# Optimization experiments

Measured on AMD Instinct MI355X. Metric: run time of the kernel, lower is better.

The kernel has to match this reference:

```python
import jax, jax.numpy as jnp
import numpy as np

N = 50000
E = 1600000
IN_DIM = 128
HIDDEN = 128


def setup_inputs() -> dict:
    key = jax.random.key(0)
    ks = jax.random.split(key, 10)
    s = lambda d: 1.0 / np.sqrt(d)
    return {
        "x": jax.random.normal(ks[0], (N, IN_DIM), dtype=jnp.float32),
        "edge_index": jax.random.randint(ks[1], (2, E), 0, N, dtype=jnp.int64),
        "w1l": jax.random.normal(ks[2], (HIDDEN, IN_DIM), dtype=jnp.float32) * s(IN_DIM),
        "b1l": jnp.zeros((HIDDEN,), dtype=jnp.float32),
        "w1r": jax.random.normal(ks[3], (HIDDEN, IN_DIM), dtype=jnp.float32) * s(IN_DIM),
        "w2l": jax.random.normal(ks[4], (HIDDEN, HIDDEN), dtype=jnp.float32) * s(HIDDEN),
        "b2l": jnp.zeros((HIDDEN,), dtype=jnp.float32),
        "w2r": jax.random.normal(ks[5], (HIDDEN, HIDDEN), dtype=jnp.float32) * s(HIDDEN),
        "mw1": jax.random.normal(ks[6], (HIDDEN, HIDDEN), dtype=jnp.float32) * s(HIDDEN),
        "mb1": jnp.zeros((HIDDEN,), dtype=jnp.float32),
        "mw2": jax.random.normal(ks[7], (1, HIDDEN), dtype=jnp.float32) * s(HIDDEN),
        "mb2": jnp.zeros((1,), dtype=jnp.float32),
    }


def _mean_aggr(x, src, dst, num_nodes):
    # scatter-mean of source features onto target nodes (PyG SAGEConv mean aggr)
    summed = jax.ops.segment_sum(x[src], dst, num_segments=num_nodes)  # [N, D]
    count = jax.ops.segment_sum(jnp.ones((src.shape[0],), x.dtype), dst,
                                num_segments=num_nodes)
    return summed / jnp.maximum(count, 1.0)[:, None]


def _sage_conv(x, src, dst, wl, bl, wr):
    # out = lin_l(mean_aggr(x_neighbors)) + lin_r(x_root)
    aggr = _mean_aggr(x, src, dst, x.shape[0])
    return aggr @ wl.T + bl + x @ wr.T


def reference(x, edge_index, w1l, b1l, w1r, w2l, b2l, w2r, mw1, mb1, mw2, mb2):
    src, dst = edge_index[0], edge_index[1]
    h = jax.nn.relu(_sage_conv(x, src, dst, w1l, b1l, w1r))   # dropout: eval mode
    h = jax.nn.relu(_sage_conv(h, src, dst, w2l, b2l, w2r))
    h = jax.nn.relu(h @ mw1.T + mb1)
    logits = (h @ mw2.T + mb2).squeeze(-1)                    # [N]
    return logits
```

## Files before the change

### kernel.cpp

```cpp
#include <hip/hip_runtime.h>
#include <hip/hip_bf16.h>
#include <cstdint>

#define HD 128
#define BKSZ 256
#define BCAP 12288

typedef __attribute__((ext_vector_type(8))) short bfx8;
typedef __attribute__((ext_vector_type(4))) float fx4;

__device__ inline float bf2f(short s) {
    union { uint32_t u; float f; } c;
    c.u = ((uint32_t)(unsigned short)s) << 16;
    return c.f;
}
__device__ inline unsigned short f2bf(float v) {
    union { float f; uint32_t u; } c;
    c.f = v;
    uint32_t u = c.u + 0x7FFF + ((c.u >> 16) & 1);
    return (unsigned short)(u >> 16);
}

__device__ inline void stage_lds(const void* g, void* l, int nbytes) {
    const char* gc = (const char*)g;
    for (int off = threadIdx.x * 16; off < nbytes; off += 4096) {
        __builtin_amdgcn_global_load_lds(
            (const __attribute__((address_space(1))) unsigned int*)(gc + off),
            (__attribute__((address_space(3))) unsigned int*)
                ((__attribute__((address_space(3))) char*)l + off),
            16, 0, 0);
    }
}


__global__ void k_zero(int* __restrict__ p, int n) {
    int i = blockIdx.x * 256 + threadIdx.x;
    if (i < n) p[i] = 0;
}

__global__ __launch_bounds__(256) void k_bin(const int* __restrict__ ei, int E, int NBK,
                                             int* __restrict__ bcnt,
                                             int* __restrict__ bpack) {
    __shared__ int lhist[BKSZ];
    __shared__ int gbase[BKSZ];
    int base = blockIdx.x * 4096;

    for (int i = threadIdx.x; i < NBK; i += 256) lhist[i] = 0;
    __syncthreads();

    int pw[16];
    int meta[16];
    const int4* s4 = (const int4*)ei;
    const int4* d4 = (const int4*)(ei + E);
    int c0 = base >> 2;
    int EC = E >> 2;
#pragma unroll
    for (int j = 0; j < 4; ++j) {
        int c4 = c0 + j * 256 + threadIdx.x;
        bool ok = (c4 < EC);
        int4 sv = make_int4(0, 0, 0, 0), dv = make_int4(0, 0, 0, 0);
        if (ok) { sv = s4[c4]; dv = d4[c4]; }
        int ss[4] = {sv.x, sv.y, sv.z, sv.w};
        int dd[4] = {dv.x, dv.y, dv.z, dv.w};
#pragma unroll
        for (int l = 0; l < 4; ++l) {
            int idx = j * 4 + l;
            meta[idx] = -1;
            if (ok) {
                int d = dd[l];
                int b = d >> 8;
                int lr = atomicAdd(&lhist[b], 1);
                pw[idx]   = ((d & 255) << 24) | ss[l];
                meta[idx] = (b << 16) | lr;
            }
        }
    }
    __syncthreads();
    for (int i = threadIdx.x; i < NBK; i += 256) {
        int c = lhist[i];
        gbase[i] = c ? atomicAdd(&bcnt[i], c) : 0;
    }
    __syncthreads();
#pragma unroll
    for (int idx = 0; idx < 16; ++idx) {
        int m = meta[idx];
        if (m >= 0) {
            int b = m >> 16, lr = m & 0xFFFF;
            int pos = b * BCAP + min(gbase[b] + lr, BCAP - 1);
            bpack[pos] = pw[idx];
        }
    }
}

__global__ __launch_bounds__(1024) void k_bscan(const int* __restrict__ bcnt,
                                                int* __restrict__ boff, int NBK, int E) {
    __shared__ int sh[1024];
    int t = threadIdx.x;
    int v = (t < NBK) ? bcnt[t] : 0;
    sh[t] = v;
    __syncthreads();
    for (int d = 1; d < 1024; d <<= 1) {
        int o = (t >= d) ? sh[t - d] : 0;
        __syncthreads();
        sh[t] += o;
        __syncthreads();
    }
    if (t < NBK) boff[t] = sh[t] - v;
    if (t == 0) boff[NBK] = E;
}

__global__ __launch_bounds__(256) void k_bucket(const int* __restrict__ bpack,
                                                const int* __restrict__ bcnt,
                                                const int* __restrict__ boff,
                                                int* __restrict__ offsets,
                                                int* __restrict__ sorted,
                                                int N, int E) {
    __shared__ int lh[BKSZ];
    __shared__ int cur[BKSZ];
    __shared__ int wsum[4];
    int b = blockIdx.x;
    int cnt = min(bcnt[b], BCAP);
    int base = b * BCAP;
    int obase = boff[b];
    int tid = threadIdx.x;

    lh[tid] = 0;
    __syncthreads();
    for (int i = tid; i < cnt; i += 256)
        atomicAdd(&lh[((unsigned)bpack[base + i]) >> 24], 1);
    __syncthreads();

    int v = lh[tid];
    int sum = v;
#pragma unroll
    for (int s = 1; s < 64; s <<= 1) {
        int o = __shfl_up(sum, s, 64);
        if ((tid & 63) >= s) sum += o;
    }
    int wid = tid >> 6;
    if ((tid & 63) == 63) wsum[wid] = sum;
    __syncthreads();
    int prefix = 0;
#pragma unroll
    for (int w = 0; w < 4; ++w)
        if (w < wid) prefix += wsum[w];
    int excl = prefix + sum - v;
    int n = b * BKSZ + tid;
    if (n < N) offsets[n] = obase + excl;
    cur[tid] = excl;
    __syncthreads();

    for (int i = tid; i < cnt; i += 256) {
        int w = bpack[base + i];
        int ln = ((unsigned)w) >> 24;
        int p = atomicAdd(&cur[ln], 1);
        sorted[obase + p] = w & 0xFFFFFF;
    }
    if (b == 0 && tid == 0) offsets[N] = E;
}


__global__ void k_cast(const float* __restrict__ in, unsigned short* __restrict__ out,
                       int n8) {
    int i = blockIdx.x * 256 + threadIdx.x;
    if (i >= n8) return;
    float4 v0 = ((const float4*)in)[i * 2];
    float4 v1 = ((const float4*)in)[i * 2 + 1];
    bfx8 o;
    o[0] = (short)f2bf(v0.x); o[1] = (short)f2bf(v0.y);
    o[2] = (short)f2bf(v0.z); o[3] = (short)f2bf(v0.w);
    o[4] = (short)f2bf(v1.x); o[5] = (short)f2bf(v1.y);
    o[6] = (short)f2bf(v1.z); o[7] = (short)f2bf(v1.w);
    *(bfx8*)(out + (size_t)i * 8) = o;
}

__global__ void k_cast5(const float* __restrict__ w0, const float* __restrict__ w1,
                        const float* __restrict__ w2, const float* __restrict__ w3,
                        const float* __restrict__ w4, unsigned short* __restrict__ out) {
    int t = blockIdx.x * 256 + threadIdx.x;
    if (t >= 5 * 2048) return;
    int m = t / 2048, s = t % 2048;
    const float* src = (m == 0) ? w0 : (m == 1) ? w1 : (m == 2) ? w2 : (m == 3) ? w3 : w4;
    int l  = s & 63;
    int fi = s >> 6;
    int kk = fi >> 3;
    int cf = fi & 7;
    int r  = l & 15;
    int hi = l >> 4;
    int row  = cf * 16 + r;
    int col0 = kk * 32 + hi * 8;
    const float4* sp = (const float4*)(src + row * HD + col0);
    float4 v0 = sp[0];
    float4 v1 = sp[1];
    bfx8 o;
    o[0] = (short)f2bf(v0.x); o[1] = (short)f2bf(v0.y);
    o[2] = (short)f2bf(v0.z); o[3] = (short)f2bf(v0.w);
    o[4] = (short)f2bf(v1.x); o[5] = (short)f2bf(v1.y);
    o[6] = (short)f2bf(v1.z); o[7] = (short)f2bf(v1.w);
    *(bfx8*)(out + (size_t)t * 8) = o;
}


__global__ __launch_bounds__(256) void k_aggr(const unsigned short* __restrict__ x,
                                              const int* __restrict__ offsets,
                                              const int* __restrict__ sorted_src,
                                              unsigned short* __restrict__ out, int N) {
    int wid  = threadIdx.x >> 6;
    int lane = threadIdx.x & 63;
    int n = blockIdx.x * 4 + wid;
    if (n >= N) return;
    int slot = lane >> 4;
    int c    = lane & 15;
    int beg = offsets[n], end = offsets[n + 1];

    float acc[8];
#pragma unroll
    for (int j = 0; j < 8; ++j) acc[j] = 0.f;

    int e = beg + slot;
    for (; e + 4 < end; e += 8) {
        int i0 = sorted_src[e];
        int i1 = sorted_src[e + 4];
        bfx8 v0 = *(const bfx8*)(x + (size_t)i0 * HD + c * 8);
        bfx8 v1 = *(const bfx8*)(x + (size_t)i1 * HD + c * 8);
#pragma unroll
        for (int j = 0; j < 8; ++j) acc[j] += bf2f(v0[j]);
#pragma unroll
        for (int j = 0; j < 8; ++j) acc[j] += bf2f(v1[j]);
    }
    if (e < end) {
        int i0 = sorted_src[e];
        bfx8 v0 = *(const bfx8*)(x + (size_t)i0 * HD + c * 8);
#pragma unroll
        for (int j = 0; j < 8; ++j) acc[j] += bf2f(v0[j]);
    }

#pragma unroll
    for (int j = 0; j < 8; ++j) {
        acc[j] += __shfl_xor(acc[j], 16, 64);
        acc[j] += __shfl_xor(acc[j], 32, 64);
    }
    if (slot == 0) {
        float inv = 1.f / fmaxf((float)(end - beg), 1.f);
        bfx8 o;
#pragma unroll
        for (int j = 0; j < 8; ++j) o[j] = (short)f2bf(acc[j] * inv);
        *(bfx8*)(out + (size_t)n * HD + c * 8) = o;
    }
}


__global__ __launch_bounds__(256) void k_gemm_mfma(
    const unsigned short* __restrict__ A,
    const unsigned short* __restrict__ B,
    const unsigned short* __restrict__ Wl,
    const unsigned short* __restrict__ Wr,
    const float* __restrict__ bias,
    unsigned short* __restrict__ outb, int nrows) {
    __shared__ bfx8 ldsW[4096];

    int wid  = threadIdx.x >> 6;
    int lane = threadIdx.x & 63;
    int r  = lane & 15;
    int hi = lane >> 4;
    int ko = hi * 8;
    int row0 = blockIdx.x * 64 + wid * 16;

    int arow  = row0 + r;
    int arowc = min(arow, nrows - 1);

    bfx8 a[4], b[4];
    const unsigned short* Ar = A + (size_t)arowc * HD;
    const unsigned short* Br = B + (size_t)arowc * HD;
#pragma unroll
    for (int kk = 0; kk < 4; ++kk) {
        a[kk] = *(const bfx8*)(Ar + kk * 32 + ko);
        b[kk] = *(const bfx8*)(Br + kk * 32 + ko);
    }

    stage_lds(Wl, &ldsW[0],    32768);
    stage_lds(Wr, &ldsW[2048], 32768);

    float bv[8];
#pragma unroll
    for (int cf = 0; cf < 8; ++cf) bv[cf] = bias[cf * 16 + r];

    fx4 acc[8];
#pragma unroll
    for (int cf = 0; cf < 8; ++cf) acc[cf] = (fx4){0.f, 0.f, 0.f, 0.f};

    __syncthreads();

#pragma unroll
    for (int kk = 0; kk < 4; ++kk) {
#pragma unroll
        for (int cf = 0; cf < 8; ++cf) {
            acc[cf] = __builtin_amdgcn_mfma_f32_16x16x32_bf16(
                a[kk], ldsW[(kk * 8 + cf) * 64 + lane], acc[cf], 0, 0, 0);
            acc[cf] = __builtin_amdgcn_mfma_f32_16x16x32_bf16(
                b[kk], ldsW[2048 + (kk * 8 + cf) * 64 + lane], acc[cf], 0, 0, 0);
        }
    }

#pragma unroll
    for (int cf = 0; cf < 8; ++cf) {
#pragma unroll
        for (int j = 0; j < 4; ++j) {
            int row = row0 + hi * 4 + j;
            if (row < nrows)
                outb[(size_t)row * HD + cf * 16 + r] = f2bf(fmaxf(acc[cf][j] + bv[cf], 0.f));
        }
    }
}


__global__ __launch_bounds__(256) void k_l2_fused(
    const unsigned short* __restrict__ A,
    const unsigned short* __restrict__ B,
    const unsigned short* __restrict__ Wl,
    const unsigned short* __restrict__ Wr,
    const float* __restrict__ bias,
    const unsigned short* __restrict__ Mw1,
    const float* __restrict__ mb1,
    const float* __restrict__ mw2,
    const float* __restrict__ mb2,
    float* __restrict__ outf, int nrows) {
    __shared__ bfx8 ldsW[4096];
    __shared__ unsigned short hlds[64 * HD];

    int wid  = threadIdx.x >> 6;
    int lane = threadIdx.x & 63;
    int r  = lane & 15;
    int hi = lane >> 4;
    int ko = hi * 8;
    int row0 = blockIdx.x * 64 + wid * 16;

    int arow  = row0 + r;
    int arowc = min(arow, nrows - 1);

    bfx8 a[4], b[4];
    const unsigned short* Ar = A + (size_t)arowc * HD;
    const unsigned short* Br = B + (size_t)arowc * HD;
#pragma unroll
    for (int kk = 0; kk < 4; ++kk) {
        a[kk] = *(const bfx8*)(Ar + kk * 32 + ko);
        b[kk] = *(const bfx8*)(Br + kk * 32 + ko);
    }

    stage_lds(Wl, &ldsW[0],    32768);
    stage_lds(Wr, &ldsW[2048], 32768);

    float bv[8];
#pragma unroll
    for (int cf = 0; cf < 8; ++cf) bv[cf] = bias[cf * 16 + r];

    fx4 acc[8];
#pragma unroll
    for (int cf = 0; cf < 8; ++cf) acc[cf] = (fx4){0.f, 0.f, 0.f, 0.f};

    __syncthreads();

#pragma unroll
    for (int kk = 0; kk < 4; ++kk) {
#pragma unroll
        for (int cf = 0; cf < 8; ++cf) {
            acc[cf] = __builtin_amdgcn_mfma_f32_16x16x32_bf16(
                a[kk], ldsW[(kk * 8 + cf) * 64 + lane], acc[cf], 0, 0, 0);
            acc[cf] = __builtin_amdgcn_mfma_f32_16x16x32_bf16(
                b[kk], ldsW[2048 + (kk * 8 + cf) * 64 + lane], acc[cf], 0, 0, 0);
        }
    }

#pragma unroll
    for (int cf = 0; cf < 8; ++cf) {
#pragma unroll
        for (int j = 0; j < 4; ++j) {
            int row_l = wid * 16 + hi * 4 + j;
            unsigned boff = (unsigned)(row_l * 256 + (cf * 16 + r) * 2);
            boff ^= (unsigned)((row_l & 7) << 4);
            *(unsigned short*)((char*)hlds + boff) = f2bf(fmaxf(acc[cf][j] + bv[cf], 0.f));
        }
    }
    __syncthreads();

    stage_lds(Mw1, &ldsW[0], 32768);

    bfx8 af[4];
    {
        int row_l = wid * 16 + r;
#pragma unroll
        for (int kk = 0; kk < 4; ++kk) {
            unsigned boff = (unsigned)(row_l * 256 + (kk * 32 + ko) * 2);
            boff ^= (unsigned)((row_l & 7) << 4);
            af[kk] = *(const bfx8*)((char*)hlds + boff);
        }
    }

    float m1v[8], m2v[8];
#pragma unroll
    for (int cf = 0; cf < 8; ++cf) {
        m1v[cf] = mb1[cf * 16 + r];
        m2v[cf] = mw2[cf * 16 + r];
    }

    fx4 acc2[8];
#pragma unroll
    for (int cf = 0; cf < 8; ++cf) acc2[cf] = (fx4){0.f, 0.f, 0.f, 0.f};

    __syncthreads();

#pragma unroll
    for (int kk = 0; kk < 4; ++kk) {
#pragma unroll
        for (int cf = 0; cf < 8; ++cf)
            acc2[cf] = __builtin_amdgcn_mfma_f32_16x16x32_bf16(
                af[kk], ldsW[(kk * 8 + cf) * 64 + lane], acc2[cf], 0, 0, 0);
    }

    float pd[4] = {0.f, 0.f, 0.f, 0.f};
#pragma unroll
    for (int cf = 0; cf < 8; ++cf) {
#pragma unroll
        for (int j = 0; j < 4; ++j)
            pd[j] += fmaxf(acc2[cf][j] + m1v[cf], 0.f) * m2v[cf];
    }

#pragma unroll
    for (int s = 1; s < 16; s <<= 1) {
#pragma unroll
        for (int j = 0; j < 4; ++j)
            pd[j] += __shfl_xor(pd[j], s, 64);
    }
    if (r == 0) {
        float mb = mb2[0];
#pragma unroll
        for (int j = 0; j < 4; ++j) {
            int row = row0 + hi * 4 + j;
            if (row < nrows) outf[row] = pd[j] + mb;
        }
    }
}


extern "C" void kernel_launch(void* const* d_in, const int* in_sizes, int n_in,
                              void* d_out, int out_size, void* d_ws, size_t ws_size,
                              hipStream_t stream) {
    const float* x   = (const float*)d_in[0];
    const int*   ei  = (const int*)d_in[1];
    const float* w1l = (const float*)d_in[2];
    const float* b1l = (const float*)d_in[3];
    const float* w1r = (const float*)d_in[4];
    const float* w2l = (const float*)d_in[5];
    const float* b2l = (const float*)d_in[6];
    const float* w2r = (const float*)d_in[7];
    const float* mw1 = (const float*)d_in[8];
    const float* mb1 = (const float*)d_in[9];
    const float* mw2 = (const float*)d_in[10];
    const float* mb2 = (const float*)d_in[11];
    float* out = (float*)d_out;

    const int N = in_sizes[0] / HD;
    const int E = in_sizes[1] / 2;
    const int NBK = (N + BKSZ - 1) / BKSZ;

    char* p = (char*)d_ws;
    auto alloc = [&](size_t bytes) -> char* {
        char* q = p;
        p += (bytes + 255) & ~(size_t)255;
        return q;
    };
    int*            bcnt    = (int*)alloc((size_t)NBK * 4);
    int*            boff    = (int*)alloc(((size_t)NBK + 1) * 4);
    int*            offsets = (int*)alloc(((size_t)N + 1) * 4);
    int*            bpack   = (int*)alloc((size_t)NBK * BCAP * 4);
    int*            sorted  = (int*)alloc((size_t)E * 4);
    unsigned short* Wtb     = (unsigned short*)alloc((size_t)5 * HD * HD * 2);
    unsigned short* xb      = (unsigned short*)alloc((size_t)N * HD * 2);
    unsigned short* bufA    = (unsigned short*)alloc((size_t)N * HD * 2);
    unsigned short* bufB    = (unsigned short*)alloc((size_t)N * HD * 2);

    const unsigned short* W1l = Wtb + 0 * HD * HD;
    const unsigned short* W1r = Wtb + 1 * HD * HD;
    const unsigned short* W2l = Wtb + 2 * HD * HD;
    const unsigned short* W2r = Wtb + 3 * HD * HD;
    const unsigned short* Mw1 = Wtb + 4 * HD * HD;

    const int eb4k = (E + 4095) / 4096;
    const int gb   = (N + 63) / 64;
    const int ab   = (N + 3) / 4;

    k_zero<<<1, 256, 0, stream>>>(bcnt, NBK);
    k_bin<<<eb4k, 256, 0, stream>>>(ei, E, NBK, bcnt, bpack);
    k_bscan<<<1, 1024, 0, stream>>>(bcnt, boff, NBK, E);
    k_bucket<<<NBK, 256, 0, stream>>>(bpack, bcnt, boff, offsets, sorted, N, E);

    k_cast<<<(N * HD / 8 + 255) / 256, 256, 0, stream>>>(x, xb, N * HD / 8);
    k_cast5<<<40, 256, 0, stream>>>(w1l, w1r, w2l, w2r, mw1, Wtb);

    k_aggr<<<ab, 256, 0, stream>>>(xb, offsets, sorted, bufA, N);
    k_gemm_mfma<<<gb, 256, 0, stream>>>(bufA, xb, W1l, W1r, b1l, bufB, N);
    k_aggr<<<ab, 256, 0, stream>>>(bufB, offsets, sorted, bufA, N);
    k_l2_fused<<<gb, 256, 0, stream>>>(bufA, bufB, W2l, W2r, b2l, Mw1, mb1, mw2, mb2,
                                       out, N);
}
```

Before: 264.9 us.

## Merge binning and casts into one front kernel; compute bucket offsets inside k_bucket

The edge-binning kernel, the feature cast and the weight cast are merged into a single launch that dispatches on block index. The separate bucket-offset scan kernel is removed. Each k_bucket block instead sums the counts of all preceding buckets with a wavefront reduction. This removes three kernel launches and their serialization gaps. In exchange every bucket block does a small redundant reduction over up to 256 counts, and the design assumes NBK is at most 256.

New measurement: 258.2 us. -2.5%, faster.

```diff
diff --git a/kernel.cpp b/kernel.cpp
--- a/kernel.cpp
+++ b/kernel.cpp
@@ -32,100 +32,133 @@
     }
 }
 
-
 __global__ void k_zero(int* __restrict__ p, int n) {
-    int i = blockIdx.x * 256 + threadIdx.x;
-    if (i < n) p[i] = 0;
-}
-
-__global__ __launch_bounds__(256) void k_bin(const int* __restrict__ ei, int E, int NBK,
-                                             int* __restrict__ bcnt,
-                                             int* __restrict__ bpack) {
+    for (int i = threadIdx.x; i < n; i += 256) p[i] = 0;
+}
+
+
+__global__ __launch_bounds__(256) void k_front(
+    const int* __restrict__ ei, int E, int NBK,
+    int* __restrict__ bcnt, int* __restrict__ bpack,
+    const float* __restrict__ x, unsigned short* __restrict__ xb, int n8,
+    const float* __restrict__ w0, const float* __restrict__ w1,
+    const float* __restrict__ w2, const float* __restrict__ w3,
+    const float* __restrict__ w4, unsigned short* __restrict__ wout,
+    int nbin, int ncast) {
     __shared__ int lhist[BKSZ];
     __shared__ int gbase[BKSZ];
-    int base = blockIdx.x * 4096;
-
-    for (int i = threadIdx.x; i < NBK; i += 256) lhist[i] = 0;
-    __syncthreads();
-
-    int pw[16];
-    int meta[16];
-    const int4* s4 = (const int4*)ei;
-    const int4* d4 = (const int4*)(ei + E);
-    int c0 = base >> 2;
-    int EC = E >> 2;
-#pragma unroll
-    for (int j = 0; j < 4; ++j) {
-        int c4 = c0 + j * 256 + threadIdx.x;
-        bool ok = (c4 < EC);
-        int4 sv = make_int4(0, 0, 0, 0), dv = make_int4(0, 0, 0, 0);
-        if (ok) { sv = s4[c4]; dv = d4[c4]; }
-        int ss[4] = {sv.x, sv.y, sv.z, sv.w};
-        int dd[4] = {dv.x, dv.y, dv.z, dv.w};
-#pragma unroll
-        for (int l = 0; l < 4; ++l) {
-            int idx = j * 4 + l;
-            meta[idx] = -1;
-            if (ok) {
-                int d = dd[l];
-                int b = d >> 8;
-                int lr = atomicAdd(&lhist[b], 1);
-                pw[idx]   = ((d & 255) << 24) | ss[l];
-                meta[idx] = (b << 16) | lr;
+
+    int bid = blockIdx.x;
+    if (bid < nbin) {
+        int base = bid * 4096;
+        for (int i = threadIdx.x; i < NBK; i += 256) lhist[i] = 0;
+        __syncthreads();
+
+        int pw[16];
+        int meta[16];
+        const int4* s4 = (const int4*)ei;
+        const int4* d4 = (const int4*)(ei + E);
+        int c0 = base >> 2;
+        int EC = E >> 2;
+#pragma unroll
+        for (int j = 0; j < 4; ++j) {
+            int c4 = c0 + j * 256 + threadIdx.x;
+            bool ok = (c4 < EC);
+            int4 sv = make_int4(0, 0, 0, 0), dv = make_int4(0, 0, 0, 0);
+            if (ok) { sv = s4[c4]; dv = d4[c4]; }
+            int ss[4] = {sv.x, sv.y, sv.z, sv.w};
+            int dd[4] = {dv.x, dv.y, dv.z, dv.w};
+#pragma unroll
+            for (int l = 0; l < 4; ++l) {
+                int idx = j * 4 + l;
+                meta[idx] = -1;
+                if (ok) {
+                    int d = dd[l];
+                    int b = d >> 8;
+                    int lr = atomicAdd(&lhist[b], 1);
+                    pw[idx]   = ((d & 255) << 24) | ss[l];
+                    meta[idx] = (b << 16) | lr;
+                }
             }
         }
-    }
-    __syncthreads();
-    for (int i = threadIdx.x; i < NBK; i += 256) {
-        int c = lhist[i];
-        gbase[i] = c ? atomicAdd(&bcnt[i], c) : 0;
-    }
-    __syncthreads();
-#pragma unroll
-    for (int idx = 0; idx < 16; ++idx) {
-        int m = meta[idx];
-        if (m >= 0) {
-            int b = m >> 16, lr = m & 0xFFFF;
-            int pos = b * BCAP + min(gbase[b] + lr, BCAP - 1);
-            bpack[pos] = pw[idx];
-        }
-    }
-}
-
-__global__ __launch_bounds__(1024) void k_bscan(const int* __restrict__ bcnt,
-                                                int* __restrict__ boff, int NBK, int E) {
-    __shared__ int sh[1024];
-    int t = threadIdx.x;
-    int v = (t < NBK) ? bcnt[t] : 0;
-    sh[t] = v;
-    __syncthreads();
-    for (int d = 1; d < 1024; d <<= 1) {
-        int o = (t >= d) ? sh[t - d] : 0;
         __syncthreads();
-        sh[t] += o;
+        for (int i = threadIdx.x; i < NBK; i += 256) {
+            int c = lhist[i];
+            gbase[i] = c ? atomicAdd(&bcnt[i], c) : 0;
+        }
         __syncthreads();
-    }
-    if (t < NBK) boff[t] = sh[t] - v;
-    if (t == 0) boff[NBK] = E;
+#pragma unroll
+        for (int idx = 0; idx < 16; ++idx) {
+            int m = meta[idx];
+            if (m >= 0) {
+                int b = m >> 16, lr = m & 0xFFFF;
+                int pos = b * BCAP + min(gbase[b] + lr, BCAP - 1);
+                bpack[pos] = pw[idx];
+            }
+        }
+    } else if (bid < nbin + ncast) {
+        int i = (bid - nbin) * 256 + threadIdx.x;
+        if (i >= n8) return;
+        float4 v0 = ((const float4*)x)[i * 2];
+        float4 v1 = ((const float4*)x)[i * 2 + 1];
+        bfx8 o;
+        o[0] = (short)f2bf(v0.x); o[1] = (short)f2bf(v0.y);
+        o[2] = (short)f2bf(v0.z); o[3] = (short)f2bf(v0.w);
+        o[4] = (short)f2bf(v1.x); o[5] = (short)f2bf(v1.y);
+        o[6] = (short)f2bf(v1.z); o[7] = (short)f2bf(v1.w);
+        *(bfx8*)(xb + (size_t)i * 8) = o;
+    } else {
+        int t = (bid - nbin - ncast) * 256 + threadIdx.x;
+        if (t >= 5 * 2048) return;
+        int m = t / 2048, s = t % 2048;
+        const float* src = (m == 0) ? w0 : (m == 1) ? w1 : (m == 2) ? w2
+                                                   : (m == 3) ? w3 : w4;
+        int l  = s & 63;
+        int fi = s >> 6;
+        int kk = fi >> 3;
+        int cf = fi & 7;
+        int r  = l & 15;
+        int hi = l >> 4;
+        int row  = cf * 16 + r;
+        int col0 = kk * 32 + hi * 8;
+        const float4* sp = (const float4*)(src + row * HD + col0);
+        float4 v0 = sp[0];
+        float4 v1 = sp[1];
+        bfx8 o;
+        o[0] = (short)f2bf(v0.x); o[1] = (short)f2bf(v0.y);
+        o[2] = (short)f2bf(v0.z); o[3] = (short)f2bf(v0.w);
+        o[4] = (short)f2bf(v1.x); o[5] = (short)f2bf(v1.y);
+        o[6] = (short)f2bf(v1.z); o[7] = (short)f2bf(v1.w);
+        *(bfx8*)(wout + (size_t)t * 8) = o;
+    }
 }
 
 __global__ __launch_bounds__(256) void k_bucket(const int* __restrict__ bpack,
                                                 const int* __restrict__ bcnt,
-                                                const int* __restrict__ boff,
                                                 int* __restrict__ offsets,
                                                 int* __restrict__ sorted,
                                                 int N, int E) {
     __shared__ int lh[BKSZ];
     __shared__ int cur[BKSZ];
     __shared__ int wsum[4];
+    __shared__ int psum[4];
     int b = blockIdx.x;
+    int tid = threadIdx.x;
+    int lane = tid & 63;
+    int wid = tid >> 6;
+
+    int pv = (tid < b) ? bcnt[tid] : 0;
+    int ps = pv;
+#pragma unroll
+    for (int s = 1; s < 64; s <<= 1) ps += __shfl_xor(ps, s, 64);
+    if (lane == 0) psum[wid] = ps;
+
     int cnt = min(bcnt[b], BCAP);
     int base = b * BCAP;
-    int obase = boff[b];
-    int tid = threadIdx.x;
-
     lh[tid] = 0;
     __syncthreads();
+    int obase = psum[0] + psum[1] + psum[2] + psum[3];
+
     for (int i = tid; i < cnt; i += 256)
         atomicAdd(&lh[((unsigned)bpack[base + i]) >> 24], 1);
     __syncthreads();
@@ -137,7 +170,6 @@
         int o = __shfl_up(sum, s, 64);
         if ((tid & 63) >= s) sum += o;
     }
-    int wid = tid >> 6;
     if ((tid & 63) == 63) wsum[wid] = sum;
     __syncthreads();
     int prefix = 0;
@@ -157,47 +189,6 @@
         sorted[obase + p] = w & 0xFFFFFF;
     }
     if (b == 0 && tid == 0) offsets[N] = E;
-}
-
-
-__global__ void k_cast(const float* __restrict__ in, unsigned short* __restrict__ out,
-                       int n8) {
-    int i = blockIdx.x * 256 + threadIdx.x;
-    if (i >= n8) return;
-    float4 v0 = ((const float4*)in)[i * 2];
-    float4 v1 = ((const float4*)in)[i * 2 + 1];
-    bfx8 o;
-    o[0] = (short)f2bf(v0.x); o[1] = (short)f2bf(v0.y);
-    o[2] = (short)f2bf(v0.z); o[3] = (short)f2bf(v0.w);
-    o[4] = (short)f2bf(v1.x); o[5] = (short)f2bf(v1.y);
-    o[6] = (short)f2bf(v1.z); o[7] = (short)f2bf(v1.w);
-    *(bfx8*)(out + (size_t)i * 8) = o;
-}
-
-__global__ void k_cast5(const float* __restrict__ w0, const float* __restrict__ w1,
-                        const float* __restrict__ w2, const float* __restrict__ w3,
-                        const float* __restrict__ w4, unsigned short* __restrict__ out) {
-    int t = blockIdx.x * 256 + threadIdx.x;
-    if (t >= 5 * 2048) return;
-    int m = t / 2048, s = t % 2048;
-    const float* src = (m == 0) ? w0 : (m == 1) ? w1 : (m == 2) ? w2 : (m == 3) ? w3 : w4;
-    int l  = s & 63;
-    int fi = s >> 6;
-    int kk = fi >> 3;
-    int cf = fi & 7;
-    int r  = l & 15;
-    int hi = l >> 4;
-    int row  = cf * 16 + r;
-    int col0 = kk * 32 + hi * 8;
-    const float4* sp = (const float4*)(src + row * HD + col0);
-    float4 v0 = sp[0];
-    float4 v1 = sp[1];
-    bfx8 o;
-    o[0] = (short)f2bf(v0.x); o[1] = (short)f2bf(v0.y);
-    o[2] = (short)f2bf(v0.z); o[3] = (short)f2bf(v0.w);
-    o[4] = (short)f2bf(v1.x); o[5] = (short)f2bf(v1.y);
-    o[6] = (short)f2bf(v1.z); o[7] = (short)f2bf(v1.w);
-    *(bfx8*)(out + (size_t)t * 8) = o;
 }
 
 
@@ -462,6 +453,7 @@
     const int N = in_sizes[0] / HD;
     const int E = in_sizes[1] / 2;
     const int NBK = (N + BKSZ - 1) / BKSZ;
+    const int n8 = N * HD / 8;
 
     char* p = (char*)d_ws;
     auto alloc = [&](size_t bytes) -> char* {
@@ -470,7 +462,6 @@
         return q;
     };
     int*            bcnt    = (int*)alloc((size_t)NBK * 4);
-    int*            boff    = (int*)alloc(((size_t)NBK + 1) * 4);
     int*            offsets = (int*)alloc(((size_t)N + 1) * 4);
     int*            bpack   = (int*)alloc((size_t)NBK * BCAP * 4);
     int*            sorted  = (int*)alloc((size_t)E * 4);
@@ -485,17 +476,17 @@
     const unsigned short* W2r = Wtb + 3 * HD * HD;
     const unsigned short* Mw1 = Wtb + 4 * HD * HD;
 
-    const int eb4k = (E + 4095) / 4096;
-    const int gb   = (N + 63) / 64;
-    const int ab   = (N + 3) / 4;
+    const int nbin  = (E + 4095) / 4096;
+    const int ncast = (n8 + 255) / 256;
+    const int nc5   = 40;
+    const int gb    = (N + 63) / 64;
+    const int ab    = (N + 3) / 4;
 
     k_zero<<<1, 256, 0, stream>>>(bcnt, NBK);
-    k_bin<<<eb4k, 256, 0, stream>>>(ei, E, NBK, bcnt, bpack);
-    k_bscan<<<1, 1024, 0, stream>>>(bcnt, boff, NBK, E);
-    k_bucket<<<NBK, 256, 0, stream>>>(bpack, bcnt, boff, offsets, sorted, N, E);
-
-    k_cast<<<(N * HD / 8 + 255) / 256, 256, 0, stream>>>(x, xb, N * HD / 8);
-    k_cast5<<<40, 256, 0, stream>>>(w1l, w1r, w2l, w2r, mw1, Wtb);
+    k_front<<<nbin + ncast + nc5, 256, 0, stream>>>(
+        ei, E, NBK, bcnt, bpack, x, xb, n8,
+        w1l, w1r, w2l, w2r, mw1, Wtb, nbin, ncast);
+    k_bucket<<<NBK, 256, 0, stream>>>(bpack, bcnt, offsets, sorted, N, E);
 
     k_aggr<<<ab, 256, 0, stream>>>(xb, offsets, sorted, bufA, N);
     k_gemm_mfma<<<gb, 256, 0, stream>>>(bufA, xb, W1l, W1r, b1l, bufB, N);
```
